# Optimization experiments

Measured on AMD Instinct MI355X. Metric: run time of the kernel, lower is better.

The kernel has to match this reference:

```python
import jax, jax.numpy as jnp
import numpy as np

B, N, C = 1, 32768, 256
NH, F, AG, P = 8, 32, 64, 4  # heads, cube side, agent tokens, pool size (P**3==AG)
HD = C // NH


def setup_inputs() -> dict:
    key = jax.random.key(0)
    ks = jax.random.split(key, 4)
    s = 0.02
    return {
        "x": jax.random.normal(ks[0], (B, N, C), jnp.float32),
        "w_qkv": jax.random.normal(ks[1], (3 * C, C), jnp.float32) * s,
        "b_qkv": jnp.zeros((3 * C,), jnp.float32),
        "w_proj": jax.random.normal(ks[2], (C, C), jnp.float32) * s,
        "b_proj": jnp.zeros((C,), jnp.float32),
        "w_dwc": jax.random.normal(ks[3], (C, C, 3, 3, 3), jnp.float32) * s,
        "b_dwc": jnp.zeros((C,), jnp.float32),
    }


def reference(x, w_qkv, b_qkv, w_proj, b_proj, w_dwc, b_dwc):
    scale = HD ** -0.5
    # qkv projection -> (3, B*NH, N, HD), replicating torch reshape/permute exactly
    qkv = x @ w_qkv.T + b_qkv                       # (B, N, 3C)
    qkv = qkv.reshape(B, N, 3, NH, HD)
    qkv = jnp.transpose(qkv, (2, 0, 3, 1, 4)).reshape(3, B * NH, N, HD)
    q, k, v = qkv[0], qkv[1], qkv[2]

    # agent tokens: pool q (note torch's raw reshape interleaves heads into channels)
    q_vol = q.reshape(B, F, F, F, C)                # faithful to torch reshape
    q_vol = jnp.transpose(q_vol, (0, 4, 1, 2, 3))   # (B, C, F, F, F)
    blk = F // P
    A = q_vol.reshape(B, C, P, blk, P, blk, P, blk).mean(axis=(3, 5, 7))  # (B,C,P,P,P)
    A = A.reshape(B, C, AG).transpose(0, 2, 1)      # (B, AG, C)
    A = A.reshape(B, AG, NH, HD).transpose(0, 2, 1, 3).reshape(B * NH, AG, HD)

    # stage 1: agents attend to keys, aggregate values
    agent_attn = jax.nn.softmax((A * scale) @ jnp.swapaxes(k, -2, -1), axis=-1)  # (B*NH, AG, N)
    agent_v = agent_attn @ v                        # (B*NH, AG, HD)
    # stage 2: queries attend to agents
    q_attn = jax.nn.softmax((q * scale) @ jnp.swapaxes(A, -2, -1), axis=-1)      # (B*NH, N, AG)
    o = q_attn @ agent_v                            # (B*NH, N, HD)

    # faithful to torch: transpose(1,2) then raw reshape
    o = jnp.swapaxes(o, 1, 2).reshape(B, N, C)

    # conv residual on v: (B*NH, N, HD) -> (B, C, F, F, F)
    v5 = jnp.swapaxes(v, 1, 2).reshape(B, C, F, F, F)
    conv = jax.lax.conv_general_dilated(
        v5, w_dwc, window_strides=(1, 1, 1), padding="SAME",
        dimension_numbers=("NCDHW", "OIDHW", "NCDHW"))
    conv = conv + b_dwc[None, :, None, None, None]
    o = o + jnp.transpose(conv, (0, 2, 3, 4, 1)).reshape(B, N, C)

    return o @ w_proj.T + b_proj
```

## Files before the change

### kernel.cpp

```cpp
#include <hip/hip_runtime.h>
#include <stdint.h>

typedef unsigned short u16;
typedef __attribute__((ext_vector_type(8))) short bf16x8;
typedef __attribute__((ext_vector_type(4))) float f32x4;

__device__ __forceinline__ u16 f2b(float f) {
  unsigned u = __float_as_uint(f);
  unsigned r = (u + 0x7fffu + ((u >> 16) & 1u)) >> 16;
  return (u16)r;
}
__device__ __forceinline__ float b2f(u16 s) { return __uint_as_float(((unsigned)s) << 16); }

__device__ __forceinline__ void async16(const void* g, void* l) {
  __builtin_amdgcn_global_load_lds((const __attribute__((address_space(1))) unsigned int*)g,
                                   (__attribute__((address_space(3))) unsigned int*)l, 16, 0, 0);
}


__global__ void cast_bf16(const float* __restrict__ src, u16* __restrict__ dst, int n4) {
  int i = blockIdx.x * 256 + threadIdx.x;
  if (i >= n4) return;
  const float4 v = ((const float4*)src)[i];
  uint2 o;
  o.x = (unsigned)f2b(v.x) | ((unsigned)f2b(v.y) << 16);
  o.y = (unsigned)f2b(v.z) | ((unsigned)f2b(v.w) << 16);
  ((uint2*)dst)[i] = o;
}

__global__ void pack_wc(const float* __restrict__ w, u16* __restrict__ Wc) {
  int o = blockIdx.x;
  __shared__ u16 lds[6912];
  for (int t = threadIdx.x; t < 6912; t += 256) lds[t] = f2b(w[o * 6912 + t]);
  __syncthreads();
  for (int idx = threadIdx.x; idx < 6912; idx += 256) {
    int tp = idx >> 8, i = idx & 255;
    Wc[o * 6912 + idx] = lds[i * 27 + tp];
  }
}

__global__ void pool_A(const u16* __restrict__ QKV, float* __restrict__ Apre) {
  int a = blockIdx.x >> 3, s = blockIdx.x & 7;
  int t = threadIdx.x, hp = t >> 5, dp = t & 31;
  int p1 = a >> 4, p2 = (a >> 2) & 3, p3 = a & 3;
  float sum = 0.f;
  for (int ui = 0; ui < 64; ++ui) {
    int u = s * 64 + ui;
    int f1 = p1 * 8 + (u >> 6);
    int f2 = p2 * 8 + ((u >> 3) & 7);
    int f3 = p3 * 8 + (u & 7);
    int vox = f1 * 1024 + f2 * 32 + f3;
    int n  = ((vox & 4095) << 3) + hp;
    int cq = ((vox >> 12) << 5) + dp;
    sum += b2f(QKV[n * 768 + cq]);
  }
  atomicAdd(&Apre[(hp * 64 + a) * 32 + dp], sum);
}

__global__ void pool_fin(const float* __restrict__ Apre, u16* __restrict__ Abf) {
  int idx = blockIdx.x * 256 + threadIdx.x;
  Abf[idx] = f2b(Apre[idx] * (0.17677669529663687f / 512.0f));
}

__global__ void pad_v(const u16* __restrict__ QKV, u16* __restrict__ v5) {
  int idx = blockIdx.x * 256 + threadIdx.x;
  int c8 = idx & 31, vox = idx >> 5;
  int z = vox / 1156, r2 = vox - z * 1156, y = r2 / 34, x = r2 - y * 34;
  bf16x8 val = {0, 0, 0, 0, 0, 0, 0, 0};
  if (z >= 1 && z <= 32 && y >= 1 && y <= 32 && x >= 1 && x <= 32) {
    int n = (z - 1) * 1024 + (y - 1) * 32 + (x - 1);
    val = *(const bf16x8*)(QKV + n * 768 + 512 + c8 * 8);
  }
  *(bf16x8*)(v5 + vox * 256 + c8 * 8) = val;
}

__global__ void s1_norm(const float* __restrict__ avac, const float* __restrict__ rsum,
                        u16* __restrict__ avt) {
  int idx = blockIdx.x * 256 + threadIdx.x;
  int h = idx >> 11, rem = idx & 2047, a = rem >> 5, d = rem & 31;
  avt[(h * 32 + d) * 64 + a] = f2b(avac[idx] / rsum[h * 64 + a]);
}


__device__ __forceinline__ void stage64(const u16* src, int row0, int ld, int k0,
                                        short* dst, int tid) {
  int wv = tid >> 6, lane = tid & 63;
  int r15 = lane & 15, kc8 = (lane >> 4) * 8;
#pragma unroll
  for (int j = 0; j < 4; ++j) {
    int p = j & 1, g = wv * 2 + (j >> 1);
    async16(src + (row0 + g * 16 + r15) * ld + k0 + p * 32 + kc8, dst + p * 4096 + g * 512);
  }
}

__device__ __forceinline__ void mfma64(const short* As, const short* Bs, int wm, int wn,
                                       int lane, f32x4 acc[4][4]) {
  const int q = lane >> 4, c = lane & 15;
  const int fo = q * 128 + c * 8;
#pragma unroll
  for (int p = 0; p < 2; ++p) {
    bf16x8 a[4], b[4];
#pragma unroll
    for (int mt = 0; mt < 4; ++mt) a[mt] = *(const bf16x8*)&As[p * 4096 + (wm * 4 + mt) * 512 + fo];
#pragma unroll
    for (int nt = 0; nt < 4; ++nt) b[nt] = *(const bf16x8*)&Bs[p * 4096 + (wn * 4 + nt) * 512 + fo];
#pragma unroll
    for (int mt = 0; mt < 4; ++mt)
#pragma unroll
      for (int nt = 0; nt < 4; ++nt)
        acc[mt][nt] = __builtin_amdgcn_mfma_f32_16x16x32_bf16(a[mt], b[nt], acc[mt][nt], 0, 0, 0);
  }
}

__global__ __launch_bounds__(256) void gemm_qkv(const u16* __restrict__ Xb,
                                                const u16* __restrict__ Wq,
                                                const float* __restrict__ bias,
                                                u16* __restrict__ QKV) {
  const int m0 = blockIdx.x * 128, n0 = blockIdx.y * 128;
  const int tid = threadIdx.x, lane = tid & 63, wv = tid >> 6;
  const int wm = wv >> 1, wn = wv & 1, q = lane >> 4, c = lane & 15;
  __shared__ short As[8192], Bs[8192];
  f32x4 acc[4][4] = {};
  for (int kb = 0; kb < 256; kb += 64) {
    stage64(Xb, m0, 256, kb, As, tid);
    stage64(Wq, n0, 256, kb, Bs, tid);
    __syncthreads();
    mfma64(As, Bs, wm, wn, lane, acc);
    __syncthreads();
  }
#pragma unroll
  for (int nt = 0; nt < 4; ++nt) {
    int col = n0 + wn * 64 + nt * 16 + c;
    float bv = bias[col];
#pragma unroll
    for (int mt = 0; mt < 4; ++mt) {
      int row = m0 + wm * 64 + mt * 16 + q * 4;
#pragma unroll
      for (int r = 0; r < 4; ++r) QKV[(row + r) * 768 + col] = f2b(acc[mt][nt][r] + bv);
    }
  }
}

__global__ __launch_bounds__(256) void gemm_conv(const u16* __restrict__ v5,
                                                 const u16* __restrict__ Wc,
                                                 const float* __restrict__ bias,
                                                 u16* __restrict__ Xp) {
  const int bid = blockIdx.x;
  const int xcd = bid & 7, idx = bid >> 3;
  const int n0 = (idx & 1) * 128;
  const int mt_i = xcd * 32 + (idx >> 1);
  const int m0 = mt_i * 128;
  const int z0 = mt_i >> 3, y0 = (mt_i & 7) * 4;
  const int tid = threadIdx.x, lane = tid & 63, wv = tid >> 6;
  const int wm = wv >> 1, wn = wv & 1, q = lane >> 4, c = lane & 15;
  const int r15 = lane & 15, kq8 = (lane >> 4) * 8;
  __shared__ short As[4608];
  __shared__ short Bs[12288];
  f32x4 acc[4][4] = {};
  const u16* browB = Wc + (n0 + r15) * 6912 + kq8;
  for (int dzy = 0; dzy < 9; ++dzy) {
    int dz = dzy / 3, dy = dzy - dz * 3;
    int base = (z0 + dz) * 1156 + (y0 + dy) * 34;
    int tap0 = dzy * 3;
    for (int panel = 0; panel < 8; ++panel) {
      int choff = panel * 32 + kq8;
      for (int g = wv; g < 9; g += 4) {
        int row = base + g * 16 + r15;
        row = row < 39303 ? row : 39303;
        async16(v5 + row * 256 + choff, As + g * 512);
      }
#pragma unroll
      for (int i = wv; i < 24; i += 4) {
        int dx = i >> 3, g = i & 7;
        async16(browB + g * (16 * 6912) + (tap0 + dx) * 256 + panel * 32, Bs + i * 512);
      }
      __syncthreads();
#pragma unroll
      for (int dx = 0; dx < 3; ++dx) {
        bf16x8 a[4], b[4];
#pragma unroll
        for (int mt = 0; mt < 4; ++mt) {
          int M = wm * 64 + mt * 16 + c;
          int vx = M + 2 * (M >> 5) + dx;
          a[mt] = *(const bf16x8*)&As[(vx >> 4) * 512 + q * 128 + (vx & 15) * 8];
        }
#pragma unroll
        for (int nt = 0; nt < 4; ++nt)
          b[nt] = *(const bf16x8*)&Bs[dx * 4096 + (wn * 4 + nt) * 512 + q * 128 + c * 8];
#pragma unroll
        for (int mt = 0; mt < 4; ++mt)
#pragma unroll
          for (int nt = 0; nt < 4; ++nt)
            acc[mt][nt] = __builtin_amdgcn_mfma_f32_16x16x32_bf16(a[mt], b[nt], acc[mt][nt], 0, 0, 0);
      }
      __syncthreads();
    }
  }
#pragma unroll
  for (int nt = 0; nt < 4; ++nt) {
    int col = n0 + wn * 64 + nt * 16 + c;
    float bv = bias[col];
#pragma unroll
    for (int mt = 0; mt < 4; ++mt) {
      int row = m0 + wm * 64 + mt * 16 + q * 4;
#pragma unroll
      for (int r = 0; r < 4; ++r) Xp[(row + r) * 256 + col] = f2b(acc[mt][nt][r] + bv);
    }
  }
}

__global__ __launch_bounds__(256) void gemm_proj(const u16* __restrict__ Xp,
                                                 const u16* __restrict__ Wp,
                                                 const float* __restrict__ bias,
                                                 float* __restrict__ out) {
  const int m0 = blockIdx.x * 128, n0 = blockIdx.y * 128;
  const int tid = threadIdx.x, lane = tid & 63, wv = tid >> 6;
  const int wm = wv >> 1, wn = wv & 1, q = lane >> 4, c = lane & 15;
  __shared__ short As[8192], Bs[8192];
  f32x4 acc[4][4] = {};
  for (int kb = 0; kb < 256; kb += 64) {
    stage64(Xp, m0, 256, kb, As, tid);
    stage64(Wp, n0, 256, kb, Bs, tid);
    __syncthreads();
    mfma64(As, Bs, wm, wn, lane, acc);
    __syncthreads();
  }
#pragma unroll
  for (int nt = 0; nt < 4; ++nt) {
    int col = n0 + wn * 64 + nt * 16 + c;
    float bv = bias[col];
#pragma unroll
    for (int mt = 0; mt < 4; ++mt) {
      int row = m0 + wm * 64 + mt * 16 + q * 4;
#pragma unroll
      for (int r = 0; r < 4; ++r) out[(row + r) * 256 + col] = acc[mt][nt][r] + bv;
    }
  }
}

__global__ __launch_bounds__(256) void s1_attn(const u16* __restrict__ QKV,
                                               const u16* __restrict__ Abf,
                                               float* __restrict__ avac,
                                               float* __restrict__ rsum) {
  const int h = blockIdx.y, n0 = blockIdx.x * 256;
  const int tid = threadIdx.x, lane = tid & 63, wv = tid >> 6;
  const int q = lane >> 4, c = lane & 15;
  extern __shared__ char smem[];
  u16* E  = (u16*)smem;
  u16* VT = (u16*)(smem + 33792);
  float* RED = (float*)smem;

  {
    const u16* vrow = QKV + (n0 + tid) * 768 + 512 + h * 32;
#pragma unroll
    for (int d8 = 0; d8 < 4; ++d8) {
      bf16x8 v = *(const bf16x8*)(vrow + d8 * 8);
#pragma unroll
      for (int e = 0; e < 8; ++e) VT[(d8 * 8 + e) * 264 + tid] = (u16)v[e];
    }
  }
  {
    bf16x8 af[4], bf[4];
#pragma unroll
    for (int mt = 0; mt < 4; ++mt)
      af[mt] = *(const bf16x8*)(Abf + h * 2048 + (mt * 16 + c) * 32 + q * 8);
#pragma unroll
    for (int nt = 0; nt < 4; ++nt)
      bf[nt] = *(const bf16x8*)(QKV + (n0 + wv * 64 + nt * 16 + c) * 768 + 256 + h * 32 + q * 8);
#pragma unroll
    for (int mt = 0; mt < 4; ++mt)
#pragma unroll
      for (int nt = 0; nt < 4; ++nt) {
        f32x4 s = {0.f, 0.f, 0.f, 0.f};
        s = __builtin_amdgcn_mfma_f32_16x16x32_bf16(af[mt], bf[nt], s, 0, 0, 0);
#pragma unroll
        for (int r = 0; r < 4; ++r) {
          int a = mt * 16 + q * 4 + r, nl = wv * 64 + nt * 16 + c;
          E[a * 264 + nl] = f2b(__expf(s[r]));
        }
      }
  }
  __syncthreads();
  {
    int a = tid >> 2, seg = tid & 3;
    float sum = 0.f;
    for (int i = 0; i < 64; ++i) sum += b2f(E[a * 264 + seg * 64 + i]);
    sum += __shfl_xor(sum, 1);
    sum += __shfl_xor(sum, 2);
    if (seg == 0) atomicAdd(&rsum[h * 64 + a], sum);
  }
  f32x4 pv[4][2] = {};
#pragma unroll
  for (int ks = 0; ks < 2; ++ks) {
    bf16x8 ap[4], bp[2];
#pragma unroll
    for (int mt = 0; mt < 4; ++mt)
      ap[mt] = *(const bf16x8*)&E[(mt * 16 + c) * 264 + wv * 64 + ks * 32 + q * 8];
#pragma unroll
    for (int nt = 0; nt < 2; ++nt)
      bp[nt] = *(const bf16x8*)&VT[(nt * 16 + c) * 264 + wv * 64 + ks * 32 + q * 8];
#pragma unroll
    for (int mt = 0; mt < 4; ++mt)
#pragma unroll
      for (int nt = 0; nt < 2; ++nt)
        pv[mt][nt] = __builtin_amdgcn_mfma_f32_16x16x32_bf16(ap[mt], bp[nt], pv[mt][nt], 0, 0, 0);
  }
  __syncthreads();
#pragma unroll
  for (int mt = 0; mt < 4; ++mt)
#pragma unroll
    for (int nt = 0; nt < 2; ++nt)
#pragma unroll
      for (int r = 0; r < 4; ++r)
        RED[wv * 2048 + (mt * 16 + q * 4 + r) * 32 + nt * 16 + c] = pv[mt][nt][r];
  __syncthreads();
  for (int idx = tid; idx < 2048; idx += 256) {
    float t = RED[idx] + RED[2048 + idx] + RED[4096 + idx] + RED[6144 + idx];
    atomicAdd(&avac[h * 2048 + idx], t);
  }
}

__global__ __launch_bounds__(256) void s2_attn(const u16* __restrict__ QKV,
                                               const u16* __restrict__ Abf,
                                               const u16* __restrict__ avt,
                                               u16* __restrict__ Xp) {
  const int h = blockIdx.y, n0 = blockIdx.x * 256;
  const int tid = threadIdx.x, lane = tid & 63, wv = tid >> 6;
  const int q = lane >> 4, c = lane & 15;
  extern __shared__ char smem[];
  u16* P = (u16*)smem;
  float* O = (float*)smem;

  f32x4 s[4][4];
  {
    bf16x8 af[4], bf[4];
#pragma unroll
    for (int mt = 0; mt < 4; ++mt)
      af[mt] = *(const bf16x8*)(QKV + (n0 + wv * 64 + mt * 16 + c) * 768 + h * 32 + q * 8);
#pragma unroll
    for (int nt = 0; nt < 4; ++nt)
      bf[nt] = *(const bf16x8*)(Abf + h * 2048 + (nt * 16 + c) * 32 + q * 8);
#pragma unroll
    for (int mt = 0; mt < 4; ++mt)
#pragma unroll
      for (int nt = 0; nt < 4; ++nt) {
        f32x4 z = {0.f, 0.f, 0.f, 0.f};
        s[mt][nt] = __builtin_amdgcn_mfma_f32_16x16x32_bf16(af[mt], bf[nt], z, 0, 0, 0);
      }
  }
#pragma unroll
  for (int mt = 0; mt < 4; ++mt)
#pragma unroll
    for (int r = 0; r < 4; ++r) {
      float v0 = s[mt][0][r], v1 = s[mt][1][r], v2 = s[mt][2][r], v3 = s[mt][3][r];
      float mx = fmaxf(fmaxf(v0, v1), fmaxf(v2, v3));
      mx = fmaxf(mx, __shfl_xor(mx, 1));
      mx = fmaxf(mx, __shfl_xor(mx, 2));
      mx = fmaxf(mx, __shfl_xor(mx, 4));
      mx = fmaxf(mx, __shfl_xor(mx, 8));
      float e0 = __expf(v0 - mx), e1 = __expf(v1 - mx), e2 = __expf(v2 - mx), e3 = __expf(v3 - mx);
      float sm = e0 + e1 + e2 + e3;
      sm += __shfl_xor(sm, 1);
      sm += __shfl_xor(sm, 2);
      sm += __shfl_xor(sm, 4);
      sm += __shfl_xor(sm, 8);
      float inv = 1.0f / sm;
      int tok = wv * 64 + mt * 16 + q * 4 + r;
      P[tok * 72 +      c] = f2b(e0 * inv);
      P[tok * 72 + 16 + c] = f2b(e1 * inv);
      P[tok * 72 + 32 + c] = f2b(e2 * inv);
      P[tok * 72 + 48 + c] = f2b(e3 * inv);
    }
  __syncthreads();
  f32x4 o[4][2] = {};
#pragma unroll
  for (int ks = 0; ks < 2; ++ks) {
    bf16x8 ap[4], bv[2];
#pragma unroll
    for (int mt = 0; mt < 4; ++mt)
      ap[mt] = *(const bf16x8*)&P[(wv * 64 + mt * 16 + c) * 72 + ks * 32 + q * 8];
#pragma unroll
    for (int nt = 0; nt < 2; ++nt)
      bv[nt] = *(const bf16x8*)(avt + h * 2048 + (nt * 16 + c) * 64 + ks * 32 + q * 8);
#pragma unroll
    for (int mt = 0; mt < 4; ++mt)
#pragma unroll
      for (int nt = 0; nt < 2; ++nt)
        o[mt][nt] = __builtin_amdgcn_mfma_f32_16x16x32_bf16(ap[mt], bv[nt], o[mt][nt], 0, 0, 0);
  }
  __syncthreads();
#pragma unroll
  for (int mt = 0; mt < 4; ++mt)
#pragma unroll
    for (int nt = 0; nt < 2; ++nt)
#pragma unroll
      for (int r = 0; r < 4; ++r)
        O[(nt * 16 + c) * 258 + wv * 64 + mt * 16 + q * 4 + r] = o[mt][nt][r];
  __syncthreads();
  for (int d = 0; d < 32; ++d) {
    int addr = (h * 32 + d) * 32768 + n0 + tid;
    Xp[addr] = f2b(b2f(Xp[addr]) + O[d * 258 + tid]);
  }
}


extern "C" void kernel_launch(void* const* d_in, const int* in_sizes, int n_in,
                              void* d_out, int out_size, void* d_ws, size_t ws_size,
                              hipStream_t stream) {
  const float* x      = (const float*)d_in[0];
  const float* w_qkv  = (const float*)d_in[1];
  const float* b_qkv  = (const float*)d_in[2];
  const float* w_proj = (const float*)d_in[3];
  const float* b_proj = (const float*)d_in[4];
  const float* w_dwc  = (const float*)d_in[5];
  const float* b_dwc  = (const float*)d_in[6];
  float* out = (float*)d_out;
  char* ws = (char*)d_ws;

  u16* Xb   = (u16*)(ws);
  u16* QKV  = (u16*)(ws + 16777216);
  u16* V5   = (u16*)(ws + 67108864);
  u16* Wc   = (u16*)(ws + 87232512);
  u16* Wqb  = (u16*)(ws + 90771456);
  u16* Wpb  = (u16*)(ws + 91164672);
  u16* Abf  = (u16*)(ws + 91295744);
  u16* AVT  = (u16*)(ws + 91328512);
  float* AVAC = (float*)(ws + 91361280);
  float* RSUM = (float*)(ws + 91426816);
  float* APRE = (float*)(ws + 91428864);
  u16* Xp = Xb;

  hipMemsetAsync(AVAC, 0, 65536 + 2048 + 65536, stream);
  cast_bf16<<<8192, 256, 0, stream>>>(x, Xb, 2097152);
  cast_bf16<<<192, 256, 0, stream>>>(w_qkv, Wqb, 49152);
  cast_bf16<<<64, 256, 0, stream>>>(w_proj, Wpb, 16384);
  pack_wc<<<256, 256, 0, stream>>>(w_dwc, Wc);
  gemm_qkv<<<dim3(256, 6), 256, 0, stream>>>(Xb, Wqb, b_qkv, QKV);
  pool_A<<<512, 256, 0, stream>>>(QKV, APRE);
  pool_fin<<<64, 256, 0, stream>>>(APRE, Abf);
  pad_v<<<4913, 256, 0, stream>>>(QKV, V5);
  s1_attn<<<dim3(128, 8), 256, 50688, stream>>>(QKV, Abf, AVAC, RSUM);
  s1_norm<<<64, 256, 0, stream>>>(AVAC, RSUM, AVT);
  gemm_conv<<<512, 256, 0, stream>>>(V5, Wc, b_dwc, Xp);
  s2_attn<<<dim3(128, 8), 256, 36864, stream>>>(QKV, Abf, AVT, Xp);
  gemm_proj<<<dim3(256, 2), 256, 0, stream>>>(Xp, Wpb, b_proj, out);
}
```

Baseline: 348.6 us.

## Fuse small kernels and register-prefetch the conv GEMM pipeline

Removes the pool_fin and pad_v kernels. The attention kernels now convert the fp32 pooled agent tokens to bf16 on the fly, and the QKV GEMM epilogue scatters V directly into a padded volume that a memset zeroes first. The two weight casts are merged into one launch. The conv GEMM is restructured to double the K panel to 64 and to prefetch the next stage through registers while the current stage computes, with a launch-bounds occupancy hint. Together these cut launch overhead and an extra pass over V, at the cost of more registers and LDS in the conv kernel, scattered 2-byte stores in the QKV epilogue, and a full memset of the padded buffer.

New measurement: 369.9 us. +6.1%, slower.

```diff
diff --git a/kernel.cpp b/kernel.cpp
--- a/kernel.cpp
+++ b/kernel.cpp
@@ -4,6 +4,8 @@
 typedef unsigned short u16;
 typedef __attribute__((ext_vector_type(8))) short bf16x8;
 typedef __attribute__((ext_vector_type(4))) float f32x4;
+
+#define KSCALE (0.17677669529663687f / 512.0f)
 
 __device__ __forceinline__ u16 f2b(float f) {
   unsigned u = __float_as_uint(f);
@@ -17,10 +19,31 @@
                                    (__attribute__((address_space(3))) unsigned int*)l, 16, 0, 0);
 }
 
+__device__ __forceinline__ bf16x8 frag8(const float* p, float k) {
+  float4 f0 = *(const float4*)p, f1 = *(const float4*)(p + 4);
+  bf16x8 v;
+  v[0] = f2b(f0.x * k); v[1] = f2b(f0.y * k); v[2] = f2b(f0.z * k); v[3] = f2b(f0.w * k);
+  v[4] = f2b(f1.x * k); v[5] = f2b(f1.y * k); v[6] = f2b(f1.z * k); v[7] = f2b(f1.w * k);
+  return v;
+}
+
 
 __global__ void cast_bf16(const float* __restrict__ src, u16* __restrict__ dst, int n4) {
   int i = blockIdx.x * 256 + threadIdx.x;
   if (i >= n4) return;
+  const float4 v = ((const float4*)src)[i];
+  uint2 o;
+  o.x = (unsigned)f2b(v.x) | ((unsigned)f2b(v.y) << 16);
+  o.y = (unsigned)f2b(v.z) | ((unsigned)f2b(v.w) << 16);
+  ((uint2*)dst)[i] = o;
+}
+
+__global__ void cast_w(const float* __restrict__ wq, const float* __restrict__ wp,
+                       u16* __restrict__ dq, u16* __restrict__ dp) {
+  int b = blockIdx.x;
+  const float* src = b < 192 ? wq : wp;
+  u16* dst = b < 192 ? dq : dp;
+  int i = (b < 192 ? b : b - 192) * 256 + threadIdx.x;
   const float4 v = ((const float4*)src)[i];
   uint2 o;
   o.x = (unsigned)f2b(v.x) | ((unsigned)f2b(v.y) << 16);
@@ -57,23 +80,6 @@
   atomicAdd(&Apre[(hp * 64 + a) * 32 + dp], sum);
 }
 
-__global__ void pool_fin(const float* __restrict__ Apre, u16* __restrict__ Abf) {
-  int idx = blockIdx.x * 256 + threadIdx.x;
-  Abf[idx] = f2b(Apre[idx] * (0.17677669529663687f / 512.0f));
-}
-
-__global__ void pad_v(const u16* __restrict__ QKV, u16* __restrict__ v5) {
-  int idx = blockIdx.x * 256 + threadIdx.x;
-  int c8 = idx & 31, vox = idx >> 5;
-  int z = vox / 1156, r2 = vox - z * 1156, y = r2 / 34, x = r2 - y * 34;
-  bf16x8 val = {0, 0, 0, 0, 0, 0, 0, 0};
-  if (z >= 1 && z <= 32 && y >= 1 && y <= 32 && x >= 1 && x <= 32) {
-    int n = (z - 1) * 1024 + (y - 1) * 32 + (x - 1);
-    val = *(const bf16x8*)(QKV + n * 768 + 512 + c8 * 8);
-  }
-  *(bf16x8*)(v5 + vox * 256 + c8 * 8) = val;
-}
-
 __global__ void s1_norm(const float* __restrict__ avac, const float* __restrict__ rsum,
                         u16* __restrict__ avt) {
   int idx = blockIdx.x * 256 + threadIdx.x;
@@ -115,7 +121,8 @@
 __global__ __launch_bounds__(256) void gemm_qkv(const u16* __restrict__ Xb,
                                                 const u16* __restrict__ Wq,
                                                 const float* __restrict__ bias,
-                                                u16* __restrict__ QKV) {
+                                                u16* __restrict__ QKV,
+                                                u16* __restrict__ v5) {
   const int m0 = blockIdx.x * 128, n0 = blockIdx.y * 128;
   const int tid = threadIdx.x, lane = tid & 63, wv = tid >> 6;
   const int wm = wv >> 1, wn = wv & 1, q = lane >> 4, c = lane & 15;
@@ -136,15 +143,23 @@
     for (int mt = 0; mt < 4; ++mt) {
       int row = m0 + wm * 64 + mt * 16 + q * 4;
 #pragma unroll
-      for (int r = 0; r < 4; ++r) QKV[(row + r) * 768 + col] = f2b(acc[mt][nt][r] + bv);
-    }
-  }
-}
-
-__global__ __launch_bounds__(256) void gemm_conv(const u16* __restrict__ v5,
-                                                 const u16* __restrict__ Wc,
-                                                 const float* __restrict__ bias,
-                                                 u16* __restrict__ Xp) {
+      for (int r = 0; r < 4; ++r) {
+        u16 val = f2b(acc[mt][nt][r] + bv);
+        QKV[(row + r) * 768 + col] = val;
+        if (col >= 512) {
+          int n = row + r;
+          int z = n >> 10, y = (n >> 5) & 31, x = n & 31;
+          v5[((z + 1) * 1156 + (y + 1) * 34 + (x + 1)) * 256 + (col - 512)] = val;
+        }
+      }
+    }
+  }
+}
+
+__global__ __launch_bounds__(256, 2) void gemm_conv(const u16* __restrict__ v5,
+                                                    const u16* __restrict__ Wc,
+                                                    const float* __restrict__ bias,
+                                                    u16* __restrict__ Xp) {
   const int bid = blockIdx.x;
   const int xcd = bid & 7, idx = bid >> 3;
   const int n0 = (idx & 1) * 128;
@@ -154,48 +169,78 @@
   const int tid = threadIdx.x, lane = tid & 63, wv = tid >> 6;
   const int wm = wv >> 1, wn = wv & 1, q = lane >> 4, c = lane & 15;
   const int r15 = lane & 15, kq8 = (lane >> 4) * 8;
-  __shared__ short As[4608];
-  __shared__ short Bs[12288];
+  __shared__ short As[9216];
+  __shared__ short Bs[24576];
   f32x4 acc[4][4] = {};
-  const u16* browB = Wc + (n0 + r15) * 6912 + kq8;
-  for (int dzy = 0; dzy < 9; ++dzy) {
-    int dz = dzy / 3, dy = dzy - dz * 3;
-    int base = (z0 + dz) * 1156 + (y0 + dy) * 34;
-    int tap0 = dzy * 3;
-    for (int panel = 0; panel < 8; ++panel) {
-      int choff = panel * 32 + kq8;
-      for (int g = wv; g < 9; g += 4) {
-        int row = base + g * 16 + r15;
-        row = row < 39303 ? row : 39303;
-        async16(v5 + row * 256 + choff, As + g * 512);
+  bf16x8 pa[5], pb[12];
+
+#define CONV_LOAD(s)                                                                   \
+  {                                                                                    \
+    int dzy = (s) >> 2, panel = (s) & 3;                                               \
+    int dz = dzy / 3, dy = dzy - dz * 3;                                               \
+    int tap0 = dzy * 3;                                                                \
+    int base = (z0 + dz) * 1156 + (y0 + dy) * 34;                                      \
+    int ch = panel * 64 + kq8;                                                         \
+    _Pragma("unroll")                                                                  \
+    for (int j = 0; j < 5; ++j) {                                                      \
+      int i = wv + j * 4;                                                              \
+      if (i < 18) {                                                                    \
+        int g = i >> 1, p = i & 1;                                                     \
+        int row = base + g * 16 + r15;                                                 \
+        row = row < 39303 ? row : 39303;                                               \
+        pa[j] = *(const bf16x8*)(v5 + row * 256 + ch + p * 32);                        \
+      }                                                                                \
+    }                                                                                  \
+    _Pragma("unroll")                                                                  \
+    for (int j = 0; j < 12; ++j) {                                                     \
+      int i = wv + j * 4;                                                              \
+      int dx = i >> 4, rem = i & 15, g = rem >> 1, p = rem & 1;                        \
+      pb[j] = *(const bf16x8*)(Wc + (n0 + g * 16 + r15) * 6912 + (tap0 + dx) * 256 +   \
+                               ch + p * 32);                                           \
+    }                                                                                  \
+  }
+
+  CONV_LOAD(0);
+  for (int step = 0; step < 36; ++step) {
+#pragma unroll
+    for (int j = 0; j < 5; ++j) {
+      int i = wv + j * 4;
+      if (i < 18) {
+        int g = i >> 1, p = i & 1;
+        *(bf16x8*)&As[g * 1024 + p * 512 + lane * 8] = pa[j];
       }
-#pragma unroll
-      for (int i = wv; i < 24; i += 4) {
-        int dx = i >> 3, g = i & 7;
-        async16(browB + g * (16 * 6912) + (tap0 + dx) * 256 + panel * 32, Bs + i * 512);
-      }
-      __syncthreads();
-#pragma unroll
-      for (int dx = 0; dx < 3; ++dx) {
+    }
+#pragma unroll
+    for (int j = 0; j < 12; ++j) {
+      int i = wv + j * 4;
+      int dx = i >> 4, rem = i & 15, g = rem >> 1, p = rem & 1;
+      *(bf16x8*)&Bs[dx * 8192 + g * 1024 + p * 512 + lane * 8] = pb[j];
+    }
+    __syncthreads();
+    if (step < 35) CONV_LOAD(step + 1);
+#pragma unroll
+    for (int dx = 0; dx < 3; ++dx)
+#pragma unroll
+      for (int s = 0; s < 2; ++s) {
         bf16x8 a[4], b[4];
 #pragma unroll
         for (int mt = 0; mt < 4; ++mt) {
           int M = wm * 64 + mt * 16 + c;
           int vx = M + 2 * (M >> 5) + dx;
-          a[mt] = *(const bf16x8*)&As[(vx >> 4) * 512 + q * 128 + (vx & 15) * 8];
+          a[mt] = *(const bf16x8*)&As[(vx >> 4) * 1024 + s * 512 + q * 128 + (vx & 15) * 8];
         }
 #pragma unroll
         for (int nt = 0; nt < 4; ++nt)
-          b[nt] = *(const bf16x8*)&Bs[dx * 4096 + (wn * 4 + nt) * 512 + q * 128 + c * 8];
+          b[nt] = *(const bf16x8*)&Bs[dx * 8192 + (wn * 4 + nt) * 1024 + s * 512 + q * 128 + c * 8];
 #pragma unroll
         for (int mt = 0; mt < 4; ++mt)
 #pragma unroll
           for (int nt = 0; nt < 4; ++nt)
             acc[mt][nt] = __builtin_amdgcn_mfma_f32_16x16x32_bf16(a[mt], b[nt], acc[mt][nt], 0, 0, 0);
       }
-      __syncthreads();
-    }
-  }
+    __syncthreads();
+  }
+#undef CONV_LOAD
 #pragma unroll
   for (int nt = 0; nt < 4; ++nt) {
     int col = n0 + wn * 64 + nt * 16 + c;
@@ -239,7 +284,7 @@
 }
 
 __global__ __launch_bounds__(256) void s1_attn(const u16* __restrict__ QKV,
-                                               const u16* __restrict__ Abf,
+                                               const float* __restrict__ Apre,
                                                float* __restrict__ avac,
                                                float* __restrict__ rsum) {
   const int h = blockIdx.y, n0 = blockIdx.x * 256;
@@ -263,7 +308,7 @@
     bf16x8 af[4], bf[4];
 #pragma unroll
     for (int mt = 0; mt < 4; ++mt)
-      af[mt] = *(const bf16x8*)(Abf + h * 2048 + (mt * 16 + c) * 32 + q * 8);
+      af[mt] = frag8(Apre + h * 2048 + (mt * 16 + c) * 32 + q * 8, KSCALE);
 #pragma unroll
     for (int nt = 0; nt < 4; ++nt)
       bf[nt] = *(const bf16x8*)(QKV + (n0 + wv * 64 + nt * 16 + c) * 768 + 256 + h * 32 + q * 8);
@@ -321,7 +366,7 @@
 }
 
 __global__ __launch_bounds__(256) void s2_attn(const u16* __restrict__ QKV,
-                                               const u16* __restrict__ Abf,
+                                               const float* __restrict__ Apre,
                                                const u16* __restrict__ avt,
                                                u16* __restrict__ Xp) {
   const int h = blockIdx.y, n0 = blockIdx.x * 256;
@@ -339,7 +384,7 @@
       af[mt] = *(const bf16x8*)(QKV + (n0 + wv * 64 + mt * 16 + c) * 768 + h * 32 + q * 8);
 #pragma unroll
     for (int nt = 0; nt < 4; ++nt)
-      bf[nt] = *(const bf16x8*)(Abf + h * 2048 + (nt * 16 + c) * 32 + q * 8);
+      bf[nt] = frag8(Apre + h * 2048 + (nt * 16 + c) * 32 + q * 8, KSCALE);
 #pragma unroll
     for (int mt = 0; mt < 4; ++mt)
 #pragma unroll
@@ -423,7 +468,6 @@
   u16* Wc   = (u16*)(ws + 87232512);
   u16* Wqb  = (u16*)(ws + 90771456);
   u16* Wpb  = (u16*)(ws + 91164672);
-  u16* Abf  = (u16*)(ws + 91295744);
   u16* AVT  = (u16*)(ws + 91328512);
   float* AVAC = (float*)(ws + 91361280);
   float* RSUM = (float*)(ws + 91426816);
@@ -431,17 +475,15 @@
   u16* Xp = Xb;
 
   hipMemsetAsync(AVAC, 0, 65536 + 2048 + 65536, stream);
+  hipMemsetAsync(V5, 0, 39304 * 256 * 2, stream);
   cast_bf16<<<8192, 256, 0, stream>>>(x, Xb, 2097152);
-  cast_bf16<<<192, 256, 0, stream>>>(w_qkv, Wqb, 49152);
-  cast_bf16<<<64, 256, 0, stream>>>(w_proj, Wpb, 16384);
+  cast_w<<<256, 256, 0, stream>>>(w_qkv, w_proj, Wqb, Wpb);
   pack_wc<<<256, 256, 0, stream>>>(w_dwc, Wc);
-  gemm_qkv<<<dim3(256, 6), 256, 0, stream>>>(Xb, Wqb, b_qkv, QKV);
+  gemm_qkv<<<dim3(256, 6), 256, 0, stream>>>(Xb, Wqb, b_qkv, QKV, V5);
   pool_A<<<512, 256, 0, stream>>>(QKV, APRE);
-  pool_fin<<<64, 256, 0, stream>>>(APRE, Abf);
-  pad_v<<<4913, 256, 0, stream>>>(QKV, V5);
-  s1_attn<<<dim3(128, 8), 256, 50688, stream>>>(QKV, Abf, AVAC, RSUM);
+  s1_attn<<<dim3(128, 8), 256, 50688, stream>>>(QKV, APRE, AVAC, RSUM);
   s1_norm<<<64, 256, 0, stream>>>(AVAC, RSUM, AVT);
   gemm_conv<<<512, 256, 0, stream>>>(V5, Wc, b_dwc, Xp);
-  s2_attn<<<dim3(128, 8), 256, 36864, stream>>>(QKV, Abf, AVT, Xp);
+  s2_attn<<<dim3(128, 8), 256, 36864, stream>>>(QKV, APRE, AVT, Xp);
   gemm_proj<<<dim3(256, 2), 256, 0, stream>>>(Xp, Wpb, b_proj, out);
 }
```
